# Optimization experiments

Hardware: AMD Instinct MI355X
Metric: run time of the kernel (lower is better)

Reference implementation:

```python
import jax, jax.numpy as jnp
import numpy as np

N, L, N_KNOTS = 512, 64, 9
N_BINS = N_KNOTS - 1
TWO_PI = 2.0 * np.pi


def _circular_conv(x, w, b):
    # x: (N,C,H,W), w: (O,C,3,3); circular (periodic) padding as used for gauge lattices
    xp = jnp.pad(x, ((0, 0), (0, 0), (1, 1), (1, 1)), mode='wrap')
    y = jax.lax.conv_general_dilated(xp, w, (1, 1), 'VALID',
                                     dimension_numbers=('NCHW', 'OIHW', 'NCHW'))
    return y + b[None, :, None, None]


def setup_inputs() -> dict:
    key = jax.random.key(0)
    k1, k2, k3 = jax.random.split(key, 3)
    x = jax.random.normal(k1, (N, L, L), dtype=jnp.float32)
    # partition the lattice into active/passive/frozen masks
    pat = (np.add.outer(np.arange(L), 2 * np.arange(L)) % 3)
    mask_active = jnp.asarray((pat == 0).astype(np.float32))
    mask_passive = jnp.asarray((pat == 1).astype(np.float32))
    mask_frozen = jnp.asarray((pat == 2).astype(np.float32))
    conv1_w = 0.1 * jax.random.normal(k2, (32, 2, 3, 3), dtype=jnp.float32)
    conv1_b = jnp.zeros((32,), jnp.float32)
    conv2_w = 0.1 * jax.random.normal(k3, (3 * N_BINS + 1, 32, 3, 3), dtype=jnp.float32)
    conv2_b = jnp.zeros((3 * N_BINS + 1,), jnp.float32)
    return {"x": x, "mask_active": mask_active, "mask_passive": mask_passive,
            "mask_frozen": mask_frozen, "conv1_w": conv1_w, "conv1_b": conv1_b,
            "conv2_w": conv2_w, "conv2_b": conv2_b}


def reference(x, mask_active, mask_passive, mask_frozen, conv1_w, conv1_b, conv2_w, conv2_b):
    nb = N_BINS
    # prepare_u1_input: frozen-masked (cos, sin) channels
    net_in = mask_frozen[None, None] * jnp.stack([jnp.cos(x), jnp.sin(x)], axis=1)  # (N,2,L,L)
    h1 = jax.nn.gelu(_circular_conv(net_in, conv1_w, conv1_b))
    net_out = _circular_conv(h1, conv2_w, conv2_b)              # (N,3nb+1,L,L)
    net_out = jnp.transpose(net_out, (0, 2, 3, 1))              # (N,L,L,3nb+1)
    w = jax.nn.softmax(net_out[..., :nb], axis=-1)
    h = jax.nn.softmax(net_out[..., nb:2 * nb], axis=-1)
    d = jax.nn.softplus(net_out[..., 2 * nb:3 * nb])
    t = net_out[..., -1]
    # circular knots on [0, 2pi]; periodic derivative: s[-1] = s[0]
    zeros = jnp.zeros(w.shape[:-1] + (1,), w.dtype)
    kx = jnp.concatenate([zeros, TWO_PI * jnp.cumsum(w, -1)], -1)   # (N,L,L,n_knots)
    ky = jnp.concatenate([zeros, TWO_PI * jnp.cumsum(h, -1)], -1)
    s = jnp.concatenate([d, d[..., :1]], -1)
    # dir = 0 (forward): x1 = active * mod(x)
    x1 = mask_active[None] * jnp.remainder(x, TWO_PI)
    # bin search over interior knots -> k in [0, nb-1]
    k = jnp.sum((x1[..., None] >= kx[..., 1:-1]).astype(jnp.int32), axis=-1)
    g = lambda a, i: jnp.take_along_axis(a, i[..., None], axis=-1)[..., 0]
    kxk, kxk1 = g(kx, k), g(kx, k + 1)
    kyk, kyk1 = g(ky, k), g(ky, k + 1)
    sk, sk1 = g(s, k), g(s, k + 1)
    wk = kxk1 - kxk
    hk = kyk1 - kyk
    slope = hk / wk
    xi = jnp.clip((x1 - kxk) / wk, 0.0, 1.0)
    om = 1.0 - xi
    # rational-quadratic spline (Durkan et al. 2019)
    den = slope + (sk1 + sk - 2.0 * slope) * xi * om
    y = kyk + hk * (slope * xi * xi + sk * xi * om) / den
    local_logJ = jnp.log(slope * slope * (sk1 * xi * xi + 2.0 * slope * xi * om + sk * om * om)) \
                 - 2.0 * jnp.log(den)
    fx1 = mask_active[None] * (y + t)              # (1-dir)*t with dir=0
    local_logJ = mask_active[None] * local_logJ
    logJ = jnp.sum(local_logJ, axis=(1, 2))
    fx = mask_active[None] * jnp.remainder(fx1, TWO_PI) + mask_passive[None] * x + mask_frozen[None] * x
    return fx, logJ
```

## Files before the change

kernel.cpp:

```cpp
#include <hip/hip_runtime.h>
#include <math.h>

#define Nn 512
#define Ld 64
#define NB 8
#define C1 32
#define C2 25

__device__ __forceinline__ float gelu_tanh(float a) {
    float a3 = a * a * a;
    float t = tanhf(0.7978845608028654f * (a + 0.044715f * a3));
    return 0.5f * a * (1.0f + t);
}

__device__ __forceinline__ float softplus_f(float v) {
    return (v > 0.0f) ? v + log1pf(expf(-v)) : log1pf(expf(v));
}

__device__ __forceinline__ float pos_mod_2pi(float v) {
    const float T = 6.2831853071795864769f;
    float r = fmodf(v, T);
    if (r < 0.0f) r += T;
    return r;
}

__global__ __launch_bounds__(256, 8) void k1_conv1_kernel(
    const float* __restrict__ x,
    const float* __restrict__ c1w, const float* __restrict__ c1b,
    float* __restrict__ h1g)
{
    __shared__ float s_cos[8 * 69];
    __shared__ float s_sin[8 * 69];

    const int tid = threadIdx.x;
    const int rb  = blockIdx.x;
    const int n   = blockIdx.y;
    const int r0k = rb * 4;
    const float* xn = x + n * 4096;

    for (int idx = tid; idx < 8 * 68; idx += 256) {
        int li = idx / 68, lj = idx - li * 68;
        int gi = (r0k - 2 + li) & 63;
        int gj = (lj - 2) & 63;
        float xv = xn[gi * 64 + gj];
        int pat = (gi + 2 * gj) % 3;
        float sv, cv;
        sincosf(xv, &sv, &cv);
        float fz = (pat == 2) ? 1.0f : 0.0f;
        s_cos[li * 69 + lj] = fz * cv;
        s_sin[li * 69 + lj] = fz * sv;
    }
    __syncthreads();

    const int gj = tid & 63, lrow = tid >> 6;
    const int gi = r0k + lrow;

    float v[18];
    #pragma unroll
    for (int di = 0; di < 3; ++di)
        #pragma unroll
        for (int dj = 0; dj < 3; ++dj) {
            int a = (lrow + 1 + di) * 69 + (gj + 1 + dj);
            v[di * 3 + dj]     = s_cos[a];
            v[9 + di * 3 + dj] = s_sin[a];
        }

    float* outp = h1g + (size_t)n * C1 * 4096 + gi * 64 + gj;
    #pragma unroll 4
    for (int c = 0; c < C1; ++c) {
        const float* w = c1w + c * 18;
        float a1 = c1b[c];
        #pragma unroll
        for (int t = 0; t < 9; ++t) {
            a1 = fmaf(v[t],     w[t],     a1);
            a1 = fmaf(v[9 + t], w[9 + t], a1);
        }
        outp[(size_t)c * 4096] = gelu_tanh(a1);
    }
}

#define K2CH 4
#define K2PLANE (14 * 64)

__global__ __launch_bounds__(256, 8) void k2_conv2_spline_kernel(
    const float* __restrict__ x, const float* __restrict__ h1g,
    const float* __restrict__ c2w, const float* __restrict__ c2b,
    float* __restrict__ out_fx, float* __restrict__ out_logJ)
{
    __shared__ float s_h1[K2CH * K2PLANE];
    __shared__ float s_red[4];

    const float TWO_PI_F = 6.2831853071795864769f;

    const int tid  = threadIdx.x;
    const int band = blockIdx.x;
    const int n    = blockIdx.y;
    const int r0   = band * 12;
    const int R    = (band == 5) ? 4 : 12;
    const int rows_l   = R + 2;
    const int n_active = (R == 12) ? 256 : 86;
    const float* xn  = x + n * 4096;
    const float* h1n = h1g + (size_t)n * C1 * 4096;

    int g3 = tid >> 6, u = tid & 63;
    int rsel  = (u >= 22) + (u >= 43);
    int ubase = (rsel == 2) ? 43 : ((rsel == 1) ? 22 : 0);
    int rr = 3 * g3 + rsel;
    int cc = 3 * (u - ubase) + rsel;
    bool is_act = (tid < n_active);
    int jm = (cc + 63) & 63, jp = (cc + 1) & 63;

    float acc[C2];
    #pragma unroll
    for (int co = 0; co < C2; ++co) acc[co] = c2b[co];

    for (int c0 = 0; c0 < C1; c0 += K2CH) {
        __syncthreads();
        int nf4 = K2CH * rows_l * 16;
        for (int f = tid; f < nf4; f += 256) {
            int c   = f / (rows_l * 16);
            int rem = f - c * (rows_l * 16);
            int r = rem >> 4, cg = rem & 15;
            int grow = (r0 - 1 + r) & 63;
            float4 src = *(const float4*)(h1n + (size_t)(c0 + c) * 4096 + grow * 64 + cg * 4);
            *(float4*)(&s_h1[c * K2PLANE + r * 64 + cg * 4]) = src;
        }
        __syncthreads();
        if (is_act) {
            #pragma unroll 1
            for (int c = 0; c < K2CH; ++c) {
                int ci = c0 + c;
                float v[9];
                #pragma unroll
                for (int di = 0; di < 3; ++di) {
                    const float* rowp = s_h1 + c * K2PLANE + (rr + di) * 64;
                    v[di * 3 + 0] = rowp[jm];
                    v[di * 3 + 1] = rowp[cc];
                    v[di * 3 + 2] = rowp[jp];
                }
                const float* wp = c2w + ci * 9;
                #pragma unroll
                for (int co = 0; co < C2; ++co) {
                    const float* w = wp + co * (C1 * 9);
                    float a2 = acc[co];
                    #pragma unroll
                    for (int t = 0; t < 9; ++t) a2 = fmaf(v[t], w[t], a2);
                    acc[co] = a2;
                }
            }
        }
    }

    float* outn = out_fx + n * 4096;
    for (int idx = tid; idx < R * 64; idx += 256) {
        int lr = idx >> 6, c = idx & 63;
        int gi = r0 + lr;
        int pat = (gi + 2 * c) % 3;
        float xv = xn[gi * 64 + c];
        if (pat != 0) outn[gi * 64 + c] = xv;
    }

    float lj_val = 0.0f;
    if (is_act) {
        int gi = r0 + rr;
        float xv = xn[gi * 64 + cc];

        float kx[NB + 1], ky[NB + 1], sar[NB + 1];
        {
            float m = acc[0];
            #pragma unroll
            for (int q = 1; q < NB; ++q) m = fmaxf(m, acc[q]);
            float e[NB], ssum = 0.0f;
            #pragma unroll
            for (int q = 0; q < NB; ++q) { e[q] = expf(acc[q] - m); ssum += e[q]; }
            float inv = TWO_PI_F / ssum;
            float run = 0.0f;
            kx[0] = 0.0f;
            #pragma unroll
            for (int q = 0; q < NB; ++q) { run += e[q]; kx[q + 1] = run * inv; }
        }
        {
            float m = acc[NB];
            #pragma unroll
            for (int q = 1; q < NB; ++q) m = fmaxf(m, acc[NB + q]);
            float e[NB], ssum = 0.0f;
            #pragma unroll
            for (int q = 0; q < NB; ++q) { e[q] = expf(acc[NB + q] - m); ssum += e[q]; }
            float inv = TWO_PI_F / ssum;
            float run = 0.0f;
            ky[0] = 0.0f;
            #pragma unroll
            for (int q = 0; q < NB; ++q) { run += e[q]; ky[q + 1] = run * inv; }
        }
        #pragma unroll
        for (int q = 0; q < NB; ++q) sar[q] = softplus_f(acc[2 * NB + q]);
        sar[NB] = sar[0];
        float t_out = acc[3 * NB];

        float x1 = pos_mod_2pi(xv);
        int k = 0;
        #pragma unroll
        for (int q = 1; q <= NB - 1; ++q) k += (x1 >= kx[q]) ? 1 : 0;

        float kxk = 0.f, kxk1 = 0.f, kyk = 0.f, kyk1 = 0.f, sk = 0.f, sk1 = 0.f;
        #pragma unroll
        for (int q = 0; q <= NB; ++q) {
            if (q == k)     { kxk = kx[q];  kyk = ky[q];  sk  = sar[q]; }
            if (q == k + 1) { kxk1 = kx[q]; kyk1 = ky[q]; sk1 = sar[q]; }
        }

        float wk = kxk1 - kxk;
        float hk = kyk1 - kyk;
        float slope = hk / wk;
        float xi = (x1 - kxk) / wk;
        xi = fminf(fmaxf(xi, 0.0f), 1.0f);
        float om = 1.0f - xi;
        float den = slope + (sk1 + sk - 2.0f * slope) * xi * om;
        float y = kyk + hk * (slope * xi * xi + sk * xi * om) / den;
        float num = slope * slope * (sk1 * xi * xi + 2.0f * slope * xi * om + sk * om * om);
        lj_val = logf(num) - 2.0f * logf(den);

        outn[gi * 64 + cc] = pos_mod_2pi(y + t_out);
    }

    float r = lj_val;
    #pragma unroll
    for (int off = 32; off > 0; off >>= 1) r += __shfl_down(r, off, 64);
    int lane = tid & 63, wv = tid >> 6;
    if (lane == 0) s_red[wv] = r;
    __syncthreads();
    if (tid == 0)
        atomicAdd(&out_logJ[n], s_red[0] + s_red[1] + s_red[2] + s_red[3]);
}

#define CHUNK 8
#define ICOLS 68
#define ISTR  69
#define IROWSMAX 16
#define HCOLS 66
#define HSTR  67
#define HPLANE 945

__global__ __launch_bounds__(256, 4) void csplaq_v4_kernel(
    const float* __restrict__ x,
    const float* __restrict__ c1w, const float* __restrict__ c1b,
    const float* __restrict__ c2w, const float* __restrict__ c2b,
    float* __restrict__ out_fx, float* __restrict__ out_logJ)
{
    __shared__ float s_cos[IROWSMAX * ISTR];
    __shared__ float s_sin[IROWSMAX * ISTR];
    __shared__ float s_h1[CHUNK * HPLANE];
    __shared__ float s_red[4];

    const float TWO_PI_F = 6.2831853071795864769f;
    const int tid  = threadIdx.x;
    const int band = blockIdx.x;
    const int n    = blockIdx.y;
    const int r0   = band * 12;
    const int R    = (band == 5) ? 4 : 12;
    const int rows_in  = R + 4;
    const int nsite_h  = (R + 2) * HCOLS;
    const int n_active = (R == 12) ? 256 : 86;
    const float* xn = x + n * Ld * Ld;

    for (int idx = tid; idx < rows_in * ICOLS; idx += 256) {
        int li = idx / ICOLS, uu = idx - li * ICOLS;
        int gi = (r0 - 2 + li) & 63;
        int gj = (uu - 2) & 63;
        float xv = xn[gi * Ld + gj];
        int pat = (gi + 2 * gj) % 3;
        float sv, cv;
        sincosf(xv, &sv, &cv);
        float fz = (pat == 2) ? 1.0f : 0.0f;
        s_cos[li * ISTR + uu] = fz * cv;
        s_sin[li * ISTR + uu] = fz * sv;
    }

    int g3 = tid >> 6, u = tid & 63;
    int rsel  = (u >= 22) + (u >= 43);
    int ubase = (rsel == 2) ? 43 : ((rsel == 1) ? 22 : 0);
    int rr = 3 * g3 + rsel;
    int cc = 3 * (u - ubase) + rsel;
    bool is_act = (tid < n_active);

    float acc[C2];
    #pragma unroll
    for (int co = 0; co < C2; ++co) acc[co] = c2b[co];

    for (int c0 = 0; c0 < C1; c0 += CHUNK) {
        __syncthreads();
        for (int s = tid; s < nsite_h; s += 256) {
            int h = s / HCOLS, j = s - h * HCOLS;
            float v[18];
            #pragma unroll
            for (int di = 0; di < 3; ++di)
                #pragma unroll
                for (int dj = 0; dj < 3; ++dj) {
                    int a = (h + di) * ISTR + (j + dj);
                    v[di * 3 + dj]     = s_cos[a];
                    v[9 + di * 3 + dj] = s_sin[a];
                }
            #pragma unroll
            for (int c = 0; c < CHUNK; ++c) {
                const float* w = c1w + (c0 + c) * 18;
                float a1 = c1b[c0 + c];
                #pragma unroll
                for (int t = 0; t < 9; ++t) {
                    a1 = fmaf(v[t],     w[t],     a1);
                    a1 = fmaf(v[9 + t], w[9 + t], a1);
                }
                s_h1[c * HPLANE + h * HSTR + j] = gelu_tanh(a1);
            }
        }
        __syncthreads();
        if (is_act) {
            #pragma unroll 1
            for (int c = 0; c < CHUNK; ++c) {
                int ci = c0 + c;
                float v[9];
                const float* hp = s_h1 + c * HPLANE + rr * HSTR + cc;
                #pragma unroll
                for (int di = 0; di < 3; ++di)
                    #pragma unroll
                    for (int dj = 0; dj < 3; ++dj)
                        v[di * 3 + dj] = hp[di * HSTR + dj];
                const float* wp = c2w + ci * 9;
                #pragma unroll
                for (int co = 0; co < C2; ++co) {
                    const float* w = wp + co * (C1 * 9);
                    float a2 = acc[co];
                    #pragma unroll
                    for (int t = 0; t < 9; ++t) a2 = fmaf(v[t], w[t], a2);
                    acc[co] = a2;
                }
            }
        }
    }

    float* outn = out_fx + n * Ld * Ld;
    for (int idx = tid; idx < R * 64; idx += 256) {
        int lr = idx >> 6, c = idx & 63;
        int gi = r0 + lr;
        int pat = (gi + 2 * c) % 3;
        float xv = xn[gi * Ld + c];
        if (pat != 0) outn[gi * Ld + c] = xv;
    }

    float lj_val = 0.0f;
    if (is_act) {
        int gi = r0 + rr;
        float xv = xn[gi * Ld + cc];
        float kx[NB + 1], ky[NB + 1], sar[NB + 1];
        {
            float m = acc[0];
            #pragma unroll
            for (int q = 1; q < NB; ++q) m = fmaxf(m, acc[q]);
            float e[NB], ssum = 0.0f;
            #pragma unroll
            for (int q = 0; q < NB; ++q) { e[q] = expf(acc[q] - m); ssum += e[q]; }
            float inv = TWO_PI_F / ssum;
            float run = 0.0f;
            kx[0] = 0.0f;
            #pragma unroll
            for (int q = 0; q < NB; ++q) { run += e[q]; kx[q + 1] = run * inv; }
        }
        {
            float m = acc[NB];
            #pragma unroll
            for (int q = 1; q < NB; ++q) m = fmaxf(m, acc[NB + q]);
            float e[NB], ssum = 0.0f;
            #pragma unroll
            for (int q = 0; q < NB; ++q) { e[q] = expf(acc[NB + q] - m); ssum += e[q]; }
            float inv = TWO_PI_F / ssum;
            float run = 0.0f;
            ky[0] = 0.0f;
            #pragma unroll
            for (int q = 0; q < NB; ++q) { run += e[q]; ky[q + 1] = run * inv; }
        }
        #pragma unroll
        for (int q = 0; q < NB; ++q) sar[q] = softplus_f(acc[2 * NB + q]);
        sar[NB] = sar[0];
        float t_out = acc[3 * NB];

        float x1 = pos_mod_2pi(xv);
        int k = 0;
        #pragma unroll
        for (int q = 1; q <= NB - 1; ++q) k += (x1 >= kx[q]) ? 1 : 0;

        float kxk = 0.f, kxk1 = 0.f, kyk = 0.f, kyk1 = 0.f, sk = 0.f, sk1 = 0.f;
        #pragma unroll
        for (int q = 0; q <= NB; ++q) {
            if (q == k)     { kxk = kx[q];  kyk = ky[q];  sk  = sar[q]; }
            if (q == k + 1) { kxk1 = kx[q]; kyk1 = ky[q]; sk1 = sar[q]; }
        }

        float wk = kxk1 - kxk;
        float hk = kyk1 - kyk;
        float slope = hk / wk;
        float xi = (x1 - kxk) / wk;
        xi = fminf(fmaxf(xi, 0.0f), 1.0f);
        float om = 1.0f - xi;
        float den = slope + (sk1 + sk - 2.0f * slope) * xi * om;
        float y = kyk + hk * (slope * xi * xi + sk * xi * om) / den;
        float num = slope * slope * (sk1 * xi * xi + 2.0f * slope * xi * om + sk * om * om);
        lj_val = logf(num) - 2.0f * logf(den);

        outn[gi * Ld + cc] = pos_mod_2pi(y + t_out);
    }

    float r = lj_val;
    #pragma unroll
    for (int off = 32; off > 0; off >>= 1) r += __shfl_down(r, off, 64);
    int lane = tid & 63, wv = tid >> 6;
    if (lane == 0) s_red[wv] = r;
    __syncthreads();
    if (tid == 0)
        atomicAdd(&out_logJ[n], s_red[0] + s_red[1] + s_red[2] + s_red[3]);
}

extern "C" void kernel_launch(void* const* d_in, const int* in_sizes, int n_in,
                              void* d_out, int out_size, void* d_ws, size_t ws_size,
                              hipStream_t stream) {
    const float* x   = (const float*)d_in[0];
    const float* c1w = (const float*)d_in[4];
    const float* c1b = (const float*)d_in[5];
    const float* c2w = (const float*)d_in[6];
    const float* c2b = (const float*)d_in[7];

    float* out_fx   = (float*)d_out;
    float* out_logJ = out_fx + (size_t)Nn * Ld * Ld;

    hipMemsetAsync(out_logJ, 0, Nn * sizeof(float), stream);

    const size_t h1_bytes = (size_t)Nn * C1 * Ld * Ld * sizeof(float);
    if (ws_size >= h1_bytes) {
        float* h1g = (float*)d_ws;
        dim3 g1(16, Nn);
        k1_conv1_kernel<<<g1, 256, 0, stream>>>(x, c1w, c1b, h1g);
        dim3 g2(6, Nn);
        k2_conv2_spline_kernel<<<g2, 256, 0, stream>>>(x, h1g, c2w, c2b, out_fx, out_logJ);
    } else {
        dim3 grid(6, Nn);
        csplaq_v4_kernel<<<grid, 256, 0, stream>>>(x, c1w, c1b, c2w, c2b, out_fx, out_logJ);
    }
}
```

Measured before the change: 397.0 us.

## Double-buffer conv2 halo loads and switch h1 to row-major channel layout

The h1 intermediate is now stored as [n][row][channel][col], so one image row holds all 32 channels contiguously. Conv2 stages four channels at a time into two alternating shared-memory buffers: global loads for the next chunk are issued into registers before the current chunk is computed, which overlaps memory latency with the FMAs. GELU uses the equivalent sigmoid form of the tanh approximation with __expf, and the occupancy hint drops from 8 to 5 waves to allow more registers. The cost is higher LDS use, more register pressure, and small numeric differences in GELU.

```diff
diff --git a/kernel.cpp b/kernel.cpp
--- a/kernel.cpp
+++ b/kernel.cpp
@@ -11,6 +11,12 @@
     float a3 = a * a * a;
     float t = tanhf(0.7978845608028654f * (a + 0.044715f * a3));
     return 0.5f * a * (1.0f + t);
+}
+
+__device__ __forceinline__ float gelu_fast(float a) {
+    float a3 = a * a * a;
+    float u2 = 1.5957691216057308f * (a + 0.044715f * a3);
+    return a / (1.0f + __expf(-u2));
 }
 
 __device__ __forceinline__ float softplus_f(float v) {
@@ -65,7 +71,7 @@
             v[9 + di * 3 + dj] = s_sin[a];
         }
 
-    float* outp = h1g + (size_t)n * C1 * 4096 + gi * 64 + gj;
+    float* outp = h1g + ((size_t)n * 64 + gi) * 2048 + gj;
     #pragma unroll 4
     for (int c = 0; c < C1; ++c) {
         const float* w = c1w + c * 18;
@@ -75,19 +81,53 @@
             a1 = fmaf(v[t],     w[t],     a1);
             a1 = fmaf(v[9 + t], w[9 + t], a1);
         }
-        outp[(size_t)c * 4096] = gelu_tanh(a1);
+        outp[(size_t)c * 64] = gelu_fast(a1);
     }
 }
 
 #define K2CH 4
-#define K2PLANE (14 * 64)
-
-__global__ __launch_bounds__(256, 8) void k2_conv2_spline_kernel(
+#define K2PLANE 896
+#define K2BUF (K2CH * K2PLANE)
+
+#define K2_COMPUTE(BUF, CBASE)                                            \
+    {                                                                     \
+        _Pragma("unroll")                                                 \
+        for (int c = 0; c < K2CH; ++c) {                                  \
+            const int eb = (BUF) + c * K2PLANE;                           \
+            float v0 = s_h1[eb + ex0];                                    \
+            float v1 = s_h1[eb + ex1];                                    \
+            float v2 = s_h1[eb + ex2];                                    \
+            float v3 = s_h1[eb + ex3];                                    \
+            float v4 = s_h1[eb + ex4];                                    \
+            float v5 = s_h1[eb + ex5];                                    \
+            float v6 = s_h1[eb + ex6];                                    \
+            float v7 = s_h1[eb + ex7];                                    \
+            float v8 = s_h1[eb + ex8];                                    \
+            const float* wpc = c2w + ((CBASE) + c) * 9;                   \
+            _Pragma("unroll")                                             \
+            for (int co = 0; co < C2; ++co) {                             \
+                const float* w = wpc + co * (C1 * 9);        \
+                float a2 = acc[co];                                       \
+                a2 = fmaf(v0, w[0], a2);                                  \
+                a2 = fmaf(v1, w[1], a2);                                  \
+                a2 = fmaf(v2, w[2], a2);                                  \
+                a2 = fmaf(v3, w[3], a2);                                  \
+                a2 = fmaf(v4, w[4], a2);                                  \
+                a2 = fmaf(v5, w[5], a2);                                  \
+                a2 = fmaf(v6, w[6], a2);                                  \
+                a2 = fmaf(v7, w[7], a2);                                  \
+                a2 = fmaf(v8, w[8], a2);                                  \
+                acc[co] = a2;                                             \
+            }                                                             \
+        }                                                                 \
+    }
+
+__global__ __launch_bounds__(256, 5) void k2_conv2_spline_kernel(
     const float* __restrict__ x, const float* __restrict__ h1g,
     const float* __restrict__ c2w, const float* __restrict__ c2b,
     float* __restrict__ out_fx, float* __restrict__ out_logJ)
 {
-    __shared__ float s_h1[K2CH * K2PLANE];
+    __shared__ float s_h1[2 * K2BUF];
     __shared__ float s_red[4];
 
     const float TWO_PI_F = 6.2831853071795864769f;
@@ -97,10 +137,9 @@
     const int n    = blockIdx.y;
     const int r0   = band * 12;
     const int R    = (band == 5) ? 4 : 12;
-    const int rows_l   = R + 2;
     const int n_active = (R == 12) ? 256 : 86;
     const float* xn  = x + n * 4096;
-    const float* h1n = h1g + (size_t)n * C1 * 4096;
+    const float* h1n = h1g + (size_t)n * 131072;
 
     int g3 = tid >> 6, u = tid & 63;
     int rsel  = (u >= 22) + (u >= 43);
@@ -110,44 +149,67 @@
     bool is_act = (tid < n_active);
     int jm = (cc + 63) & 63, jp = (cc + 1) & 63;
 
+    const int ex0 = rr * 64 + jm, ex1 = rr * 64 + cc, ex2 = rr * 64 + jp;
+    const int ex3 = ex0 + 64,  ex4 = ex1 + 64,  ex5 = ex2 + 64;
+    const int ex6 = ex0 + 128, ex7 = ex1 + 128, ex8 = ex2 + 128;
+
+    const int q  = tid & 63;
+    const int rA = tid >> 6;
+    const int cP = q >> 4;
+    const int qq = (q & 15) << 2;
+    const float* gA = h1n + (size_t)((r0 - 1 + rA     ) & 63) * 2048 + (q << 2);
+    const float* gB = h1n + (size_t)((r0 - 1 + rA + 4 ) & 63) * 2048 + (q << 2);
+    const float* gC = h1n + (size_t)((r0 - 1 + rA + 8 ) & 63) * 2048 + (q << 2);
+    const float* gD = h1n + (size_t)((r0 - 1 + rA + 12) & 63) * 2048 + (q << 2);
+    const int iA = cP * K2PLANE + (rA     ) * 64 + qq;
+    const int iB = cP * K2PLANE + (rA + 4 ) * 64 + qq;
+    const int iC = cP * K2PLANE + (rA + 8 ) * 64 + qq;
+    const int iD = cP * K2PLANE + (rA + 12) * 64 + qq;
+    const bool st3 = (tid < 128);
+
     float acc[C2];
     #pragma unroll
     for (int co = 0; co < C2; ++co) acc[co] = c2b[co];
 
-    for (int c0 = 0; c0 < C1; c0 += K2CH) {
+    float4 sA = *(const float4*)(gA);
+    float4 sB = *(const float4*)(gB);
+    float4 sC = *(const float4*)(gC);
+    float4 sD = make_float4(0.f, 0.f, 0.f, 0.f);
+    if (st3) sD = *(const float4*)(gD);
+    *(float4*)(&s_h1[iA]) = sA;
+    *(float4*)(&s_h1[iB]) = sB;
+    *(float4*)(&s_h1[iC]) = sC;
+    if (st3) *(float4*)(&s_h1[iD]) = sD;
+    __syncthreads();
+
+    #pragma unroll 1
+    for (int c0 = 0; c0 < C1; c0 += 2 * K2CH) {
+        const int cn = c0 + K2CH;
+        sA = *(const float4*)(gA + cn * 64);
+        sB = *(const float4*)(gB + cn * 64);
+        sC = *(const float4*)(gC + cn * 64);
+        if (st3) sD = *(const float4*)(gD + cn * 64);
+        if (is_act) K2_COMPUTE(0, c0)
+        *(float4*)(&s_h1[K2BUF + iA]) = sA;
+        *(float4*)(&s_h1[K2BUF + iB]) = sB;
+        *(float4*)(&s_h1[K2BUF + iC]) = sC;
+        if (st3) *(float4*)(&s_h1[K2BUF + iD]) = sD;
         __syncthreads();
-        int nf4 = K2CH * rows_l * 16;
-        for (int f = tid; f < nf4; f += 256) {
-            int c   = f / (rows_l * 16);
-            int rem = f - c * (rows_l * 16);
-            int r = rem >> 4, cg = rem & 15;
-            int grow = (r0 - 1 + r) & 63;
-            float4 src = *(const float4*)(h1n + (size_t)(c0 + c) * 4096 + grow * 64 + cg * 4);
-            *(float4*)(&s_h1[c * K2PLANE + r * 64 + cg * 4]) = src;
-        }
-        __syncthreads();
-        if (is_act) {
-            #pragma unroll 1
-            for (int c = 0; c < K2CH; ++c) {
-                int ci = c0 + c;
-                float v[9];
-                #pragma unroll
-                for (int di = 0; di < 3; ++di) {
-                    const float* rowp = s_h1 + c * K2PLANE + (rr + di) * 64;
-                    v[di * 3 + 0] = rowp[jm];
-                    v[di * 3 + 1] = rowp[cc];
-                    v[di * 3 + 2] = rowp[jp];
-                }
-                const float* wp = c2w + ci * 9;
-                #pragma unroll
-                for (int co = 0; co < C2; ++co) {
-                    const float* w = wp + co * (C1 * 9);
-                    float a2 = acc[co];
-                    #pragma unroll
-                    for (int t = 0; t < 9; ++t) a2 = fmaf(v[t], w[t], a2);
-                    acc[co] = a2;
-                }
-            }
+
+        const int cm = c0 + 2 * K2CH;
+        if (cm < C1) {
+            sA = *(const float4*)(gA + cm * 64);
+            sB = *(const float4*)(gB + cm * 64);
+            sC = *(const float4*)(gC + cm * 64);
+            if (st3) sD = *(const float4*)(gD + cm * 64);
+        }
+        if (is_act) K2_COMPUTE(K2BUF, cn)
+        if (cm < C1) {
+            *(float4*)(&s_h1[iA]) = sA;
+            *(float4*)(&s_h1[iB]) = sB;
+            *(float4*)(&s_h1[iC]) = sC;
+            if (st3) *(float4*)(&s_h1[iD]) = sD;
+            __syncthreads();
         }
     }
 
@@ -169,44 +231,44 @@
         {
             float m = acc[0];
             #pragma unroll
-            for (int q = 1; q < NB; ++q) m = fmaxf(m, acc[q]);
+            for (int qi = 1; qi < NB; ++qi) m = fmaxf(m, acc[qi]);
             float e[NB], ssum = 0.0f;
             #pragma unroll
-            for (int q = 0; q < NB; ++q) { e[q] = expf(acc[q] - m); ssum += e[q]; }
+            for (int qi = 0; qi < NB; ++qi) { e[qi] = expf(acc[qi] - m); ssum += e[qi]; }
             float inv = TWO_PI_F / ssum;
             float run = 0.0f;
             kx[0] = 0.0f;
             #pragma unroll
-            for (int q = 0; q < NB; ++q) { run += e[q]; kx[q + 1] = run * inv; }
+            for (int qi = 0; qi < NB; ++qi) { run += e[qi]; kx[qi + 1] = run * inv; }
         }
         {
             float m = acc[NB];
             #pragma unroll
-            for (int q = 1; q < NB; ++q) m = fmaxf(m, acc[NB + q]);
+            for (int qi = 1; qi < NB; ++qi) m = fmaxf(m, acc[NB + qi]);
             float e[NB], ssum = 0.0f;
             #pragma unroll
-            for (int q = 0; q < NB; ++q) { e[q] = expf(acc[NB + q] - m); ssum += e[q]; }
+            for (int qi = 0; qi < NB; ++qi) { e[qi] = expf(acc[NB + qi] - m); ssum += e[qi]; }
             float inv = TWO_PI_F / ssum;
             float run = 0.0f;
             ky[0] = 0.0f;
             #pragma unroll
-            for (int q = 0; q < NB; ++q) { run += e[q]; ky[q + 1] = run * inv; }
-        }
-        #pragma unroll
-        for (int q = 0; q < NB; ++q) sar[q] = softplus_f(acc[2 * NB + q]);
+            for (int qi = 0; qi < NB; ++qi) { run += e[qi]; ky[qi + 1] = run * inv; }
+        }
+        #pragma unroll
+        for (int qi = 0; qi < NB; ++qi) sar[qi] = softplus_f(acc[2 * NB + qi]);
         sar[NB] = sar[0];
         float t_out = acc[3 * NB];
 
         float x1 = pos_mod_2pi(xv);
         int k = 0;
         #pragma unroll
-        for (int q = 1; q <= NB - 1; ++q) k += (x1 >= kx[q]) ? 1 : 0;
+        for (int qi = 1; qi <= NB - 1; ++qi) k += (x1 >= kx[qi]) ? 1 : 0;
 
         float kxk = 0.f, kxk1 = 0.f, kyk = 0.f, kyk1 = 0.f, sk = 0.f, sk1 = 0.f;
         #pragma unroll
-        for (int q = 0; q <= NB; ++q) {
-            if (q == k)     { kxk = kx[q];  kyk = ky[q];  sk  = sar[q]; }
-            if (q == k + 1) { kxk1 = kx[q]; kyk1 = ky[q]; sk1 = sar[q]; }
+        for (int qi = 0; qi <= NB; ++qi) {
+            if (qi == k)     { kxk = kx[qi];  kyk = ky[qi];  sk  = sar[qi]; }
+            if (qi == k + 1) { kxk1 = kx[qi]; kyk1 = ky[qi]; sk1 = sar[qi]; }
         }
 
         float wk = kxk1 - kxk;
```

New measurement: 581.1 us. +46.4%, slower.
